# Performance work log

Measured on AMD Instinct MI355X. Metric: run time of the kernel, lower is better.

Reference implementation:

```python
import jax, jax.numpy as jnp
import numpy as np

B, L, H, LAT, V = 4096, 16, 256, 64, 800


def setup_inputs() -> dict:
    key = jax.random.key(0)
    ks = jax.random.split(key, 20)
    s = 0.05
    return {
        'wid': jax.random.randint(ks[0], (B, L), 0, V),
        'tree_vec': jax.random.normal(ks[1], (B, LAT), jnp.float32),
        'emb': jax.random.normal(ks[2], (V, H), jnp.float32) * s,
        'Wz_w': jax.random.normal(ks[3], (H, 2 * H), jnp.float32) * s,
        'Wz_b': jnp.zeros((H,), jnp.float32),
        'Wr_w': jax.random.normal(ks[4], (H, H), jnp.float32) * s,
        'Ur_w': jax.random.normal(ks[5], (H, H), jnp.float32) * s,
        'Ur_b': jnp.zeros((H,), jnp.float32),
        'Wh_w': jax.random.normal(ks[6], (H, 2 * H), jnp.float32) * s,
        'Wh_b': jnp.zeros((H,), jnp.float32),
        'W_w': jax.random.normal(ks[7], (H, LAT + H), jnp.float32) * s,
        'W_b': jnp.zeros((H,), jnp.float32),
        'U_w': jax.random.normal(ks[8], (H, LAT + 2 * H), jnp.float32) * s,
        'U_b': jnp.zeros((H,), jnp.float32),
        'Wo_w': jax.random.normal(ks[9], (V, H), jnp.float32) * s,
        'Wo_b': jnp.zeros((V,), jnp.float32),
        'Us_w': jax.random.normal(ks[10], (1, H), jnp.float32) * s,
        'Us_b': jnp.zeros((1,), jnp.float32),
    }


def _decoder(wid, tree_vec, emb, Wz_w, Wz_b, Wr_w, Ur_w, Ur_b, Wh_w, Wh_b,
             W_w, W_b, U_w, U_b, Wo_w, Wo_b, Us_w, Us_b):
    nB, nL = wid.shape
    x = emb[wid]                      # [B,L,H] node embeddings
    xt = jnp.transpose(x, (1, 0, 2))  # [L,B,H]

    def gru_scan(src_seq, dst_seq):
        # JTNN GRUUpdate along a chain: carry = (m_prev, rm_prev)
        def step(carry, xs):
            m_prev, rm_prev = carry
            x_src, x_dst = xs
            z = jax.nn.sigmoid(jnp.concatenate([x_src, m_prev], -1) @ Wz_w.T + Wz_b)
            h_til = jnp.tanh(jnp.concatenate([x_src, rm_prev], -1) @ Wh_w.T + Wh_b)
            m = (1.0 - z) * m_prev + z * h_til
            r = jax.nn.sigmoid(x_dst @ Wr_w.T + m @ Ur_w.T + Ur_b)
            return (m, r * m), m
        z0 = jnp.zeros((src_seq.shape[1], H), src_seq.dtype)
        _, m_seq = jax.lax.scan(step, (z0, z0), (src_seq, dst_seq))
        return m_seq  # [L-1,B,H]

    # forward edges t->t+1 (DFS forward), reverse edges t+1->t (DFS backtrack)
    m_fwd = gru_scan(xt[:-1], xt[1:])
    m_rev = gru_scan(xt[1:][::-1], xt[:-1][::-1])[::-1]  # indexed by t

    zeros_h = jnp.zeros((nB, H), x.dtype)
    tvL = lambda n: jnp.broadcast_to(tree_vec, (n, nB, LAT))

    # p_inputs = [x_v, h_v, tree_vec] at root, each fwd step, each rev step
    p_root = jnp.concatenate([x[:, 0], zeros_h, tree_vec], -1)[None]
    p_fwd = jnp.concatenate([xt[1:], m_fwd, tvL(nL - 1)], -1)
    m_fwd_shift = jnp.concatenate([zeros_h[None], m_fwd[:-1]], 0)
    h_rev = m_fwd_shift + m_rev  # node t after backtrack pull
    p_rev = jnp.concatenate([xt[:-1], h_rev, tvL(nL - 1)], -1)[::-1]
    p_in = jnp.concatenate([p_root, p_fwd, p_rev], 0).reshape(-1, 2 * H + LAT)
    # targets: forward expansions -> 1, backtracks + final stop -> 0
    p_t = jnp.concatenate([jnp.ones((nL - 1,)), jnp.zeros((nL,))])
    p_t = jnp.broadcast_to(p_t[:, None], (2 * nL - 1, nB)).reshape(-1)

    # q_inputs = [h, tree_vec] at root and each newly created node
    q_root = jnp.concatenate([zeros_h, tree_vec], -1)[None]
    q_new = jnp.concatenate([m_fwd, tvL(nL - 1)], -1)
    q_in = jnp.concatenate([q_root, q_new], 0).reshape(-1, H + LAT)
    q_t = jnp.transpose(wid, (1, 0)).reshape(-1)  # [L*B], step-major like q_in

    q = jax.nn.relu(q_in @ W_w.T + W_b) @ Wo_w.T + Wo_b  # [L*B, V]
    p = (jax.nn.relu(p_in @ U_w.T + U_b) @ Us_w.T + Us_b)[:, 0]

    p_loss = jnp.sum(jnp.logaddexp(0.0, p) - p * p_t) / nB
    logZ = jax.nn.logsumexp(q, axis=-1)
    q_sel = jnp.take_along_axis(q, q_t[:, None], axis=1)[:, 0]
    q_loss = jnp.sum(logZ - q_sel) / nB
    p_acc = jnp.mean(((p > 0).astype(jnp.int32) == p_t.astype(jnp.int32)).astype(jnp.float32))
    q_acc = jnp.mean((jnp.argmax(q, axis=-1) == q_t).astype(jnp.float32))
    return (q_loss, p_loss, q_acc, p_acc)


def reference(wid, tree_vec, emb, Wz_w, Wz_b, Wr_w, Ur_w, Ur_b, Wh_w, Wh_b,
              W_w, W_b, U_w, U_b, Wo_w, Wo_b, Us_w, Us_b):
    return _decoder(wid, tree_vec, emb, Wz_w, Wz_b, Wr_w, Ur_w, Ur_b, Wh_w, Wh_b,
                    W_w, W_b, U_w, U_b, Wo_w, Wo_b, Us_w, Us_b)
```

## Files before the change

kernel.cpp:

```cpp
#include <hip/hip_runtime.h>
#include <math.h>


typedef unsigned short u16;
typedef __attribute__((ext_vector_type(4))) float f4;
typedef __attribute__((ext_vector_type(4))) unsigned short u16x4;
typedef __attribute__((ext_vector_type(8))) unsigned short u16x8;
typedef __attribute__((ext_vector_type(8))) short s16x8;
typedef __attribute__((ext_vector_type(4))) float f32x4;

#define DEV static __device__ __forceinline__

DEV u16 f2b(float f) {
  unsigned u = __float_as_uint(f);
  u += 0x7fffu + ((u >> 16) & 1u);
  return (u16)(u >> 16);
}
DEV float b2f(u16 h) { return __uint_as_float(((unsigned)h) << 16); }
DEV void split2(float v, u16& hi, u16& lo) {
  hi = f2b(v);
  lo = f2b(v - b2f(hi));
}
DEV float fsig(float x) { return __builtin_amdgcn_rcpf(1.f + __expf(-x)); }
DEV float ftanh(float x) {
  const float e = __expf(2.f * x);
  return 1.f - 2.f * __builtin_amdgcn_rcpf(e + 1.f);
}

DEV void gld16(const void* g, void* l) {
  __builtin_amdgcn_global_load_lds((const __attribute__((address_space(1))) void*)g,
                                   (__attribute__((address_space(3))) void*)l, 16, 0, 0);
}

#define MFMA(a, b, c) __builtin_amdgcn_mfma_f32_16x16x32_bf16((a), (b), (c), 0, 0, 0)

template <int GR, int GC, bool ASPL, bool BSPL>
DEV void mm128(const u16* __restrict__ Ah, const u16* __restrict__ Al,
               const u16* __restrict__ Bh, const u16* __restrict__ Bl,
               int K, u16* sm, f32x4* acc) {
  constexpr int MT = 8 / GR, NT = 8 / GC;
  const int tid = threadIdx.x;
  const int lane = tid & 63;
  const int wv = tid >> 6;
  const int wr = wv / GC, wc = wv % GC;
  const size_t rs = (size_t)K * 2;
  const size_t soff = (size_t)(tid >> 2) * rs + (size_t)((tid & 3) * 16);
  const char* gAh = (const char*)Ah + soff;
  const char* gBh = (const char*)Bh + soff;
  const char* gAl = nullptr;
  const char* gBl = nullptr;
  if constexpr (ASPL) gAl = (const char*)Al + soff;
  if constexpr (BSPL) gBl = (const char*)Bl + soff;
  char* L = (char*)sm;
  const int wb = wv * 1024;
  const int frow = lane & 15, fkb = (lane >> 4) * 16;
  const char* rA = L + (size_t)((wr * 16 * MT + frow) * 64 + fkb);
  const char* rB = L + 8192 + (size_t)((wc * 16 * NT + frow) * 64 + fkb);
  const size_t rskip = rs * 64;
  const int nk = K >> 5;
  for (int kt = 0; kt < nk; ++kt) {
    gld16(gAh, L + wb);
    gld16(gAh + rskip, L + 4096 + wb);
    gld16(gBh, L + 8192 + wb);
    gld16(gBh + rskip, L + 12288 + wb);
    if constexpr (ASPL) {
      gld16(gAl, L + 16384 + wb);
      gld16(gAl + rskip, L + 20480 + wb);
    }
    if constexpr (BSPL) {
      gld16(gBl, L + 24576 + wb);
      gld16(gBl + rskip, L + 28672 + wb);
    }
    gAh += 64; gBh += 64;
    if constexpr (ASPL) gAl += 64;
    if constexpr (BSPL) gBl += 64;
    __syncthreads();
    s16x8 a_[MT], b_[NT];
#pragma unroll
    for (int i = 0; i < MT; ++i) a_[i] = *(const s16x8*)(rA + i * 1024);
#pragma unroll
    for (int j = 0; j < NT; ++j) b_[j] = *(const s16x8*)(rB + j * 1024);
#pragma unroll
    for (int i = 0; i < MT; ++i)
#pragma unroll
      for (int j = 0; j < NT; ++j)
        acc[i * NT + j] = MFMA(a_[i], b_[j], acc[i * NT + j]);
    if constexpr (BSPL) {
      s16x8 bl_[NT];
#pragma unroll
      for (int j = 0; j < NT; ++j) bl_[j] = *(const s16x8*)(rB + 16384 + j * 1024);
#pragma unroll
      for (int i = 0; i < MT; ++i)
#pragma unroll
        for (int j = 0; j < NT; ++j)
          acc[i * NT + j] = MFMA(a_[i], bl_[j], acc[i * NT + j]);
    }
    if constexpr (ASPL) {
      s16x8 al_[MT];
#pragma unroll
      for (int i = 0; i < MT; ++i) al_[i] = *(const s16x8*)(rA + 16384 + i * 1024);
#pragma unroll
      for (int i = 0; i < MT; ++i)
#pragma unroll
        for (int j = 0; j < NT; ++j)
          acc[i * NT + j] = MFMA(al_[i], b_[j], acc[i * NT + j]);
    }
    __syncthreads();
  }
}

__global__ __launch_bounds__(256) void k_pack(const float* __restrict__ Wz, const float* __restrict__ Wr,
                                              const float* __restrict__ Ur, const float* __restrict__ Wh,
                                              const float* __restrict__ Ww, const float* __restrict__ Uw,
                                              const float* __restrict__ Wo, const float* __restrict__ emb,
                                              const float* __restrict__ tree,
                                              u16* wpk, u16* uzh, u16* urw, u16* wu, u16* wt2, u16* wov,
                                              u16* uxp2, u16* utp2, u16* embp, u16* tre2) {
  const int i = blockIdx.x * 256 + threadIdx.x;
  const int seg = blockIdx.y;
  u16 h, l;
  if (seg == 0) {
    if (i >= 196608) return;
    const int row = i >> 8, c = i & 255;
    const float v = (row < 256) ? Wz[row * 512 + c]
                                : (row < 512) ? Wh[(row - 256) * 512 + c] : Wr[(row - 512) * 256 + c];
    split2(v, h, l); wpk[i] = h; wpk[196608 + i] = l;
  } else if (seg == 1) {
    if (i >= 131072) return;
    const int row = i >> 8, c = i & 255;
    const float v = (row < 256) ? Wz[row * 512 + 256 + c] : Wh[(row - 256) * 512 + 256 + c];
    uzh[i] = f2b(v);
  } else if (seg == 2) {
    if (i >= 65536) return;
    urw[i] = f2b(Ur[i]);
  } else if (seg == 3) {
    if (i >= 81920) return;
    if (i < 65536) {
      const int row = i >> 8, c = i & 255;
      wu[i] = f2b(Ww[row * 320 + c]);
    } else {
      const int j = i - 65536, row = j >> 6, c = j & 63;
      split2(Ww[row * 320 + 256 + c], h, l); wt2[j] = h; wt2[16384 + j] = l;
    }
  } else if (seg == 4) {
    if (i >= 229376) return;
    const float v = (i < 204800) ? Wo[i] : 0.f;
    wov[i] = f2b(v);
  } else if (seg == 5) {
    if (i >= 147456) return;
    if (i < 65536) {
      const int row = i >> 8, c = i & 255;
      split2(Uw[row * 576 + c], h, l); uxp2[i] = h; uxp2[65536 + i] = l;
    } else if (i < 131072) {
      const int j = i - 65536, row = j >> 8, c = j & 255;
      wu[65536 + j] = f2b(Uw[row * 576 + 256 + c]);
    } else {
      const int j = i - 131072, row = j >> 6, c = j & 63;
      split2(Uw[row * 576 + 512 + c], h, l); utp2[j] = h; utp2[16384 + j] = l;
    }
  } else if (seg == 6) {
    if (i >= 229376) return;
    const int row = i >> 8;
    const float v = (row < 800) ? emb[i] : 0.f;
    split2(v, h, l); embp[i] = h; embp[229376 + i] = l;
  } else {
    if (i >= 65536) return;
    const int b = i >> 4, c4 = (i & 15) << 2;
    const f4 tv = *(const f4*)(tree + (size_t)b * 64 + c4);
    u16x4 hi, lo;
#pragma unroll
    for (int k = 0; k < 4; ++k) { u16 hh, ll; split2(tv[k], hh, ll); hi[k] = hh; lo[k] = ll; }
    *(u16x4*)(tre2 + (size_t)b * 64 + c4) = hi;
    *(u16x4*)(tre2 + 262144 + (size_t)b * 64 + c4) = lo;
  }
}

__global__ __launch_bounds__(256) void k_prep(const u16* __restrict__ embp, const u16* __restrict__ wpk,
                                              const u16* __restrict__ tre2, const u16* __restrict__ wt2,
                                              const u16* __restrict__ utp2, const u16* __restrict__ uxp2,
                                              u16* __restrict__ Aembh, float* __restrict__ Tq,
                                              float* __restrict__ Tp, float* __restrict__ Xp) {
  __shared__ u16 sm[16384];
  f32x4 acc[16] = {};
  const int bid = blockIdx.x;
  int seg, bx, by, K;
  const u16 *A0, *B0;
  size_t Aoff, Boff;
  if (bid < 42) { seg = 0; bx = bid % 7; by = bid / 7; A0 = embp; Aoff = 229376; B0 = wpk; Boff = 196608; K = 256; }
  else if (bid < 106) { const int l2 = bid - 42; seg = 1; bx = l2 % 32; by = l2 / 32; A0 = tre2; Aoff = 262144; B0 = wt2; Boff = 16384; K = 64; }
  else if (bid < 170) { const int l2 = bid - 106; seg = 2; bx = l2 % 32; by = l2 / 32; A0 = tre2; Aoff = 262144; B0 = utp2; Boff = 16384; K = 64; }
  else { const int l2 = bid - 170; seg = 3; bx = l2 % 7; by = l2 / 7; A0 = embp; Aoff = 229376; B0 = uxp2; Boff = 65536; K = 256; }
  A0 += (size_t)bx * 128 * K;
  B0 += (size_t)by * 128 * K;
  mm128<2, 2, true, true>(A0, A0 + Aoff, B0, B0 + Boff, K, sm, acc);
  const int lane = threadIdx.x & 63, wv = threadIdx.x >> 6;
  const int wr = wv >> 1, wc = wv & 1, quad = lane >> 4, c = lane & 15;
#pragma unroll
  for (int i = 0; i < 4; ++i)
#pragma unroll
    for (int j = 0; j < 4; ++j)
#pragma unroll
      for (int rg = 0; rg < 4; ++rg) {
        const size_t row = (size_t)bx * 128 + wr * 64 + i * 16 + quad * 4 + rg;
        const int col = by * 128 + wc * 64 + j * 16 + c;
        const float v = acc[i * 4 + j][rg];
        if (seg == 0) Aembh[row * 768 + col] = f2b(v);
        else if (seg == 1) Tq[row * 256 + col] = v;
        else if (seg == 2) Tp[row * 256 + col] = v;
        else Xp[row * 256 + col] = v;
      }
}

__global__ __launch_bounds__(1024, 1) void k_scan(const u16* __restrict__ uzh, const u16* __restrict__ urw,
                                                  const u16* __restrict__ Aembh, const int* __restrict__ wid,
                                                  const float* __restrict__ Wz_b, const float* __restrict__ Wh_b,
                                                  const float* __restrict__ Ur_b,
                                                  u16* __restrict__ mfh, u16* __restrict__ mrh) {
  __shared__ __align__(16) u16 MH[8192];
  __shared__ __align__(16) u16 ML[8192];
  __shared__ __align__(16) u16 RH[8192];
  __shared__ __align__(16) u16 RL[8192];
  const int tid = threadIdx.x;
  const int wv = tid >> 6, lane = tid & 63;
  const int l15 = lane & 15, quad = lane >> 4;
  const int r0 = blockIdx.x * 32;
  const int dir = r0 >> 12;
  const int b0 = r0 & 4095;
  for (int i = tid; i < 8192; i += 1024) { MH[i] = 0; ML[i] = 0; RH[i] = 0; RL[i] = 0; }
  const int zc0 = wv * 16;
  const int cc = zc0 + l15;
  const float bzv = Wz_b[cc], bhv = Wh_b[cc], urv = Ur_b[cc];
  s16x8 wz[8], wh[8];
#pragma unroll
  for (int kc = 0; kc < 8; ++kc) {
    const size_t zo = (size_t)cc * 256 + kc * 32 + quad * 8;
    wz[kc] = *(const s16x8*)(uzh + zo);
    wh[kc] = *(const s16x8*)(uzh + zo + 65536);
  }
  float mnew[2][4];
  __syncthreads();
  for (int s = 0; s < 15; ++s) {
    const int tsrc = dir ? (15 - s) : s;
    const int tdst = dir ? (14 - s) : (s + 1);
    int xids[8], xds[8];
#pragma unroll
    for (int mt = 0; mt < 2; ++mt)
#pragma unroll
      for (int rg = 0; rg < 4; ++rg) {
        const int b = b0 + mt * 16 + quad * 4 + rg;
        xids[mt * 4 + rg] = wid[b * 16 + tsrc];
        xds[mt * 4 + rg] = (s < 14) ? wid[b * 16 + tdst] : 0;
      }
    f32x4 aZ[2] = {};
    f32x4 aH[2] = {};
    for (int kc = 0; kc < 8; ++kc) {
      s16x8 amh[2], aml[2], arh[2], arl[2];
#pragma unroll
      for (int mt = 0; mt < 2; ++mt) {
        const int ai = ((kc * 4 + quad) * 32 + mt * 16 + l15) * 8;
        amh[mt] = *(const s16x8*)&MH[ai];
        aml[mt] = *(const s16x8*)&ML[ai];
        arh[mt] = *(const s16x8*)&RH[ai];
        arl[mt] = *(const s16x8*)&RL[ai];
      }
#pragma unroll
      for (int mt = 0; mt < 2; ++mt) {
        aZ[mt] = MFMA(amh[mt], wz[kc], aZ[mt]);
        aZ[mt] = MFMA(aml[mt], wz[kc], aZ[mt]);
        aH[mt] = MFMA(arh[mt], wh[kc], aH[mt]);
        aH[mt] = MFMA(arl[mt], wh[kc], aH[mt]);
      }
    }
    __syncthreads();
#pragma unroll
    for (int mt = 0; mt < 2; ++mt)
#pragma unroll
      for (int rg = 0; rg < 4; ++rg) {
        const int rr = mt * 16 + quad * 4 + rg;
        const int xid = xids[mt * 4 + rg];
        const int mi = ((cc >> 3) * 32 + rr) * 8 + (cc & 7);
        const float az = b2f(Aembh[(size_t)xid * 768 + cc]);
        const float ah = b2f(Aembh[(size_t)xid * 768 + 256 + cc]);
        const float mp = b2f(MH[mi]) + b2f(ML[mi]);
        const float z = fsig(aZ[mt][rg] + az + bzv);
        const float ht = ftanh(aH[mt][rg] + ah + bhv);
        const float mv = (1.f - z) * mp + z * ht;
        mnew[mt][rg] = mv;
        u16 hh, ll; split2(mv, hh, ll);
        MH[mi] = hh; ML[mi] = ll;
      }
    __syncthreads();
    {
      u16* dst = dir ? (mrh + ((size_t)(14 - s) * 4096 + b0) * 256)
                     : (mfh + ((size_t)s * 4096 + b0) * 256);
      const int r = tid >> 5, cg = tid & 31;
      const s16x8 v = *(const s16x8*)&MH[(cg * 32 + r) * 8];
      *(s16x8*)(dst + r * 256 + cg * 8) = v;
    }
    if (s == 14) break;
    f32x4 aR[2] = {};
    for (int kc = 0; kc < 8; ++kc) {
      s16x8 amh[2], aml[2];
#pragma unroll
      for (int mt = 0; mt < 2; ++mt) {
        const int ai = ((kc * 4 + quad) * 32 + mt * 16 + l15) * 8;
        amh[mt] = *(const s16x8*)&MH[ai];
        aml[mt] = *(const s16x8*)&ML[ai];
      }
      const size_t ro = (size_t)cc * 256 + kc * 32 + quad * 8;
      const s16x8 brh = *(const s16x8*)(urw + ro);
#pragma unroll
      for (int mt = 0; mt < 2; ++mt) {
        aR[mt] = MFMA(amh[mt], brh, aR[mt]);
        aR[mt] = MFMA(aml[mt], brh, aR[mt]);
      }
    }
#pragma unroll
    for (int mt = 0; mt < 2; ++mt)
#pragma unroll
      for (int rg = 0; rg < 4; ++rg) {
        const int rr = mt * 16 + quad * 4 + rg;
        const int xd = xds[mt * 4 + rg];
        const int mi = ((cc >> 3) * 32 + rr) * 8 + (cc & 7);
        const float ar = b2f(Aembh[(size_t)xd * 768 + 512 + cc]);
        const float rp = aR[mt][rg] + ar + urv;
        const float rmv = fsig(rp) * mnew[mt][rg];
        u16 hh, ll; split2(rmv, hh, ll);
        RH[mi] = hh; RL[mi] = ll;
      }
    __syncthreads();
  }
}

__global__ __launch_bounds__(256) void k_mid(const u16* __restrict__ mfh, const u16* __restrict__ mrh,
                                             const u16* __restrict__ wu,
                                             const float* __restrict__ Tq, const float* __restrict__ W_b,
                                             const float* __restrict__ Xp, const float* __restrict__ Tp,
                                             const float* __restrict__ U_b, const float* __restrict__ Us_w,
                                             const int* __restrict__ wid,
                                             u16* __restrict__ hq, u16* __restrict__ hrev,
                                             float* __restrict__ ppart) {
  const int bid = blockIdx.x;
  const int tid = threadIdx.x;
  if (bid < 1920) {
    __shared__ u16 sm[8192];
    f32x4 acc[16] = {};
    const int rb = bid >> 2, ct = bid & 3;
    const u16* Ah = mfh + (size_t)rb * 128 * 256;
    const u16* Bh = wu + (size_t)ct * 128 * 256;
    mm128<4, 1, false, false>(Ah, nullptr, Bh, nullptr, 256, sm, acc);
    const int lane = tid & 63, wv = tid >> 6, quad = lane >> 4, c = lane & 15;
    if (ct < 2) {
      const int colb = ct * 128;
#pragma unroll
      for (int i = 0; i < 2; ++i)
#pragma unroll
        for (int rg = 0; rg < 4; ++rg) {
          const size_t row = (size_t)rb * 128 + wv * 32 + i * 16 + quad * 4 + rg;
          const int b = (int)(row & 4095);
#pragma unroll
          for (int j = 0; j < 8; ++j) {
            const int col = colb + j * 16 + c;
            const float hv = fmaxf(acc[i * 8 + j][rg] + Tq[(size_t)b * 256 + col] + W_b[col], 0.f);
            hq[(row + 4096) * 256 + col] = f2b(hv);
          }
        }
    } else {
      const int colb = (ct - 2) * 128;
#pragma unroll
      for (int i = 0; i < 2; ++i)
#pragma unroll
        for (int rg = 0; rg < 4; ++rg) {
          const size_t row = (size_t)rb * 128 + wv * 32 + i * 16 + quad * 4 + rg;
          const int t = (int)(row >> 12), b = (int)(row & 4095);
          const int xid = wid[b * 16 + t + 1];
          const int prow = (int)row + 4096;
          float d = 0.f;
#pragma unroll
          for (int j = 0; j < 8; ++j) {
            const int col = colb + j * 16 + c;
            float h = acc[i * 8 + j][rg] + Xp[(size_t)xid * 256 + col] + Tp[(size_t)b * 256 + col] + U_b[col];
            h = fmaxf(h, 0.f);
            d += h * Us_w[col];
          }
#pragma unroll
          for (int dd = 1; dd < 16; dd <<= 1) d += __shfl_xor(d, dd);
          if (c == 0) ppart[(size_t)prow * 2 + (ct - 2)] = d;
        }
    }
  } else if (bid < 9600) {
    const int idx = (bid - 1920) * 256 + tid;
    const int r = idx >> 5, g8 = idx & 31;
    const int t = r >> 12;
    const size_t o = (size_t)r * 256 + g8 * 8;
    const u16x8 a = *(const u16x8*)(mrh + o);
    u16x8 out = a;
    if (t > 0) {
      const u16x8 a2 = *(const u16x8*)(mfh + o - 1048576);
#pragma unroll
      for (int k = 0; k < 8; ++k) out[k] = f2b(b2f(a[k]) + b2f(a2[k]));
    }
    *(u16x8*)(hrev + o) = out;
  } else {
    const int b = bid - 9600;
    const int col = tid;
    const float hv = fmaxf(Tq[(size_t)b * 256 + col] + W_b[col], 0.f);
    hq[(size_t)b * 256 + col] = f2b(hv);
    const int xid = wid[b * 16];
    float d = fmaxf(Xp[(size_t)xid * 256 + col] + Tp[(size_t)b * 256 + col] + U_b[col], 0.f) * Us_w[col];
#pragma unroll
    for (int dd = 1; dd < 64; dd <<= 1) d += __shfl_xor(d, dd);
    __shared__ float red[4];
    if ((tid & 63) == 0) red[tid >> 6] = d;
    __syncthreads();
    if (tid == 0) {
      ppart[(size_t)b * 2] = red[0] + red[1] + red[2] + red[3];
      ppart[(size_t)b * 2 + 1] = 0.f;
    }
  }
}

__global__ __launch_bounds__(256) void k_tail(const u16* __restrict__ hq, const u16* __restrict__ wov,
                                              const u16* __restrict__ wu, const u16* __restrict__ hrev,
                                              const float* __restrict__ Wo_b, const float* __restrict__ Xp,
                                              const float* __restrict__ Tp, const float* __restrict__ U_b,
                                              const float* __restrict__ Us_w, const int* __restrict__ wid,
                                              float* __restrict__ qpart, float* __restrict__ ppart) {
  __shared__ __align__(16) u16 smem[40960];
  const int bid = blockIdx.x;
  const int tid = threadIdx.x, lane = tid & 63, wv = tid >> 6;
  const int quad = lane >> 4, c = lane & 15;
  if (bid < 512) {
    char* LA = (char*)smem;
    char* LB = (char*)(smem + 32768);
    const u16* Ah = hq + (size_t)bid * 128 * 256;
    const size_t soff = (size_t)(tid >> 2) * 512 + (size_t)((tid & 3) * 16);
#pragma unroll
    for (int kt = 0; kt < 8; ++kt) {
      gld16((const char*)Ah + soff + kt * 64, LA + kt * 8192 + wv * 1024);
      gld16((const char*)Ah + soff + 32768 + kt * 64, LA + kt * 8192 + 4096 + wv * 1024);
    }
    gld16((const char*)wov + soff, LB + wv * 1024);
    gld16((const char*)wov + soff + 32768, LB + 4096 + wv * 1024);
    float rM[8], rS[8], rSel[8];
    int rAm[8], qts[8];
#pragma unroll
    for (int mt = 0; mt < 2; ++mt)
#pragma unroll
      for (int rg = 0; rg < 4; ++rg) {
        const int r8 = mt * 4 + rg;
        rM[r8] = -1e30f; rS[r8] = 0.f; rSel[r8] = -1e30f; rAm[r8] = 0x7fffffff;
        const size_t row = (size_t)bid * 128 + wv * 32 + mt * 16 + quad * 4 + rg;
        qts[r8] = wid[(row & 4095) * 16 + (int)(row >> 12)];
      }
    f32x4 acc[16];
    for (int nt = 0; nt < 7; ++nt) {
#pragma unroll
      for (int i = 0; i < 16; ++i) acc[i] = (f32x4){0.f, 0.f, 0.f, 0.f};
      for (int kt = 0; kt < 8; ++kt) {
        const int g = nt * 8 + kt;
        __syncthreads();
        if (g < 55) {
          const int nn = (g + 1) >> 3, nk = (g + 1) & 7;
          const char* Bn = (const char*)(wov + (size_t)nn * 32768) + soff + nk * 64;
          gld16(Bn, LB + ((g + 1) & 1) * 8192 + wv * 1024);
          gld16(Bn + 32768, LB + ((g + 1) & 1) * 8192 + 4096 + wv * 1024);
        }
        s16x8 af[2], bf[8];
#pragma unroll
        for (int mt = 0; mt < 2; ++mt)
          af[mt] = *(const s16x8*)(LA + kt * 8192 + (wv * 32 + mt * 16 + c) * 64 + quad * 16);
#pragma unroll
        for (int j = 0; j < 8; ++j)
          bf[j] = *(const s16x8*)(LB + (g & 1) * 8192 + (j * 16 + c) * 64 + quad * 16);
#pragma unroll
        for (int mt = 0; mt < 2; ++mt)
#pragma unroll
          for (int j = 0; j < 8; ++j)
            acc[mt * 8 + j] = MFMA(af[mt], bf[j], acc[mt * 8 + j]);
      }
      const int colb = nt * 128;
#pragma unroll
      for (int mt = 0; mt < 2; ++mt)
#pragma unroll
        for (int rg = 0; rg < 4; ++rg) {
          const int r8 = mt * 4 + rg;
          float vals[8];
          float mx = -1e30f;
          int am = 0x7fffffff;
#pragma unroll
          for (int j = 0; j < 8; ++j) {
            const int col = colb + j * 16 + c;
            float v = -1e30f;
            if (col < 800) v = acc[mt * 8 + j][rg] + Wo_b[col];
            vals[j] = v;
            if (v > mx) { mx = v; am = col; }
          }
          float gm = mx;
          int ga = am;
#pragma unroll
          for (int d = 1; d < 16; d <<= 1) {
            const float om = __shfl_xor(gm, d);
            const int oa = __shfl_xor(ga, d);
            if (om > gm || (om == gm && oa < ga)) { gm = om; ga = oa; }
          }
          float s = 0.f, sel = -1e30f;
#pragma unroll
          for (int j = 0; j < 8; ++j) {
            s += __expf(vals[j] - gm);
            if (colb + j * 16 + c == qts[r8]) sel = vals[j];
          }
#pragma unroll
          for (int d = 1; d < 16; d <<= 1) {
            s += __shfl_xor(s, d);
            sel = fmaxf(sel, __shfl_xor(sel, d));
          }
          const float oM = rM[r8];
          if (gm > oM || (gm == oM && ga < rAm[r8])) rAm[r8] = ga;
          const float nM = fmaxf(oM, gm);
          rS[r8] = rS[r8] * __expf(oM - nM) + s * __expf(gm - nM);
          rM[r8] = nM;
          rSel[r8] = fmaxf(rSel[r8], sel);
        }
    }
    if (c == 0) {
#pragma unroll
      for (int mt = 0; mt < 2; ++mt)
#pragma unroll
        for (int rg = 0; rg < 4; ++rg) {
          const int r8 = mt * 4 + rg;
          const size_t row = (size_t)bid * 128 + wv * 32 + mt * 16 + quad * 4 + rg;
          f4 o;
          o.x = rM[r8]; o.y = rS[r8]; o.z = (float)rAm[r8]; o.w = rSel[r8];
          *(f4*)(qpart + row * 4) = o;
        }
    }
  } else {
    f32x4 acc[16] = {};
    const int l2 = bid - 512;
    const int by = l2 & 1, bx = l2 >> 1;
    const u16* Ah = hrev + (size_t)bx * 128 * 256;
    const u16* Bh = wu + (size_t)(256 + by * 128) * 256;
    mm128<4, 1, false, false>(Ah, nullptr, Bh, nullptr, 256, smem, acc);
    const int colb = by * 128;
#pragma unroll
    for (int i = 0; i < 2; ++i)
#pragma unroll
      for (int rg = 0; rg < 4; ++rg) {
        const size_t row = (size_t)bx * 128 + wv * 32 + i * 16 + quad * 4 + rg;
        const int t = (int)(row >> 12), b = (int)(row & 4095);
        const int xid = wid[b * 16 + t];
        const int prow = (30 - t) * 4096 + b;
        float d = 0.f;
#pragma unroll
        for (int j = 0; j < 8; ++j) {
          const int col = colb + j * 16 + c;
          float h = acc[i * 8 + j][rg] + Xp[(size_t)xid * 256 + col] + Tp[(size_t)b * 256 + col] + U_b[col];
          h = fmaxf(h, 0.f);
          d += h * Us_w[col];
        }
#pragma unroll
        for (int dd = 1; dd < 16; dd <<= 1) d += __shfl_xor(d, dd);
        if (c == 0) ppart[(size_t)prow * 2 + by] = d;
      }
  }
}

__global__ __launch_bounds__(256) void k_red(const float* __restrict__ qpart, const float* __restrict__ ppart,
                                             const int* __restrict__ wid, const float* __restrict__ Us_b,
                                             float* __restrict__ accb) {
  __shared__ float s0, s1;
  if (threadIdx.x == 0) { s0 = 0.f; s1 = 0.f; }
  __syncthreads();
  if (blockIdx.x < 256) {
    const int r = blockIdx.x * 256 + threadIdx.x;
    const f4 p4 = *(const f4*)(qpart + (size_t)r * 4);
    const float logZ = p4.x + logf(p4.y);
    const int am = (int)p4.z;
    const int t = r >> 12, b = r & 4095;
    const int qt = wid[b * 16 + t];
    atomicAdd(&s0, logZ - p4.w);
    atomicAdd(&s1, (am == qt) ? 1.f : 0.f);
    __syncthreads();
    if (threadIdx.x == 0) {
      atomicAdd(&accb[blockIdx.x & 15], s0);
      atomicAdd(&accb[16 + (blockIdx.x & 15)], s1);
    }
  } else {
    const int r = (blockIdx.x - 256) * 256 + threadIdx.x;
    const float p = ppart[(size_t)r * 2] + ppart[(size_t)r * 2 + 1] + Us_b[0];
    const int sidx = r >> 12;
    const float pt = (sidx < 15) ? 1.f : 0.f;
    const float loss = fmaxf(p, 0.f) + log1pf(expf(-fabsf(p))) - p * pt;
    const float hit = ((p > 0.f) == (pt > 0.5f)) ? 1.f : 0.f;
    atomicAdd(&s0, loss);
    atomicAdd(&s1, hit);
    __syncthreads();
    if (threadIdx.x == 0) {
      atomicAdd(&accb[32 + (blockIdx.x & 15)], s0);
      atomicAdd(&accb[48 + (blockIdx.x & 15)], s1);
    }
  }
}

__global__ void k_finalize(const float* __restrict__ accb, float* __restrict__ out) {
  if (threadIdx.x == 0 && blockIdx.x == 0) {
    float ql = 0, qa = 0, pl = 0, pa = 0;
    for (int i = 0; i < 16; ++i) {
      ql += accb[i];
      qa += accb[16 + i];
      pl += accb[32 + i];
      pa += accb[48 + i];
    }
    out[0] = ql / 4096.f;
    out[1] = pl / 4096.f;
    out[2] = qa / 65536.f;
    out[3] = pa / 126976.f;
  }
}

__global__ void k_flag(float* __restrict__ out) {
  if (threadIdx.x < 4) out[threadIdx.x] = -12345.f;
}

extern "C" void kernel_launch(void* const* d_in, const int* in_sizes, int n_in,
                              void* d_out, int out_size, void* d_ws, size_t ws_size,
                              hipStream_t stream) {
  (void)in_sizes; (void)n_in; (void)out_size;
  const int* wid = (const int*)d_in[0];
  const float* tree = (const float*)d_in[1];
  const float* emb = (const float*)d_in[2];
  const float* Wz_w = (const float*)d_in[3];
  const float* Wz_b = (const float*)d_in[4];
  const float* Wr_w = (const float*)d_in[5];
  const float* Ur_w = (const float*)d_in[6];
  const float* Ur_b = (const float*)d_in[7];
  const float* Wh_w = (const float*)d_in[8];
  const float* Wh_b = (const float*)d_in[9];
  const float* W_w = (const float*)d_in[10];
  const float* W_b = (const float*)d_in[11];
  const float* U_w = (const float*)d_in[12];
  const float* U_b = (const float*)d_in[13];
  const float* Wo_w = (const float*)d_in[14];
  const float* Wo_b = (const float*)d_in[15];
  const float* Us_w = (const float*)d_in[16];
  const float* Us_b = (const float*)d_in[17];
  char* ws = (char*)d_ws;

  constexpr size_t NEED = 152273152ull;
  if (ws_size < NEED) {
    k_flag<<<1, 64, 0, stream>>>((float*)d_out);
    return;
  }

  u16* hq = (u16*)(ws + 0ull);
  u16* hrev = (u16*)(ws + 33554432ull);
  u16* mfh = (u16*)(ws + 65011712ull);
  u16* mrh = (u16*)(ws + 96468992ull);
  u16* Aembh = (u16*)(ws + 127926272ull);
  u16* embp = (u16*)(ws + 129302528ull);
  u16* wpk = (u16*)(ws + 130220032ull);
  u16* uzh = (u16*)(ws + 131006464ull);
  u16* urw = (u16*)(ws + 131268608ull);
  u16* wu = (u16*)(ws + 131399680ull);
  u16* wt2 = (u16*)(ws + 131661824ull);
  u16* wov = (u16*)(ws + 131727360ull);
  u16* uxp2 = (u16*)(ws + 132186112ull);
  u16* utp2 = (u16*)(ws + 132448256ull);
  u16* tre2 = (u16*)(ws + 132513792ull);
  float* Tq = (float*)(ws + 133562368ull);
  float* Tp = (float*)(ws + 137756672ull);
  float* Xp = (float*)(ws + 141950976ull);
  float* qpart = (float*)(ws + 142868480ull);
  float* ppart = (float*)(ws + 151257088ull);
  float* accb = (float*)(ws + 152272896ull);

  hipMemsetAsync(accb, 0, 256, stream);

  k_pack<<<dim3(896, 8), 256, 0, stream>>>(Wz_w, Wr_w, Ur_w, Wh_w, W_w, U_w, Wo_w, emb, tree,
                                           wpk, uzh, urw, wu, wt2, wov, uxp2, utp2, embp, tre2);
  k_prep<<<184, 256, 0, stream>>>(embp, wpk, tre2, wt2, utp2, uxp2, Aembh, Tq, Tp, Xp);
  k_scan<<<256, 1024, 0, stream>>>(uzh, urw, Aembh, wid, Wz_b, Wh_b, Ur_b, mfh, mrh);
  k_mid<<<13696, 256, 0, stream>>>(mfh, mrh, wu, Tq, W_b, Xp, Tp, U_b, Us_w, wid, hq, hrev, ppart);
  k_tail<<<1472, 256, 0, stream>>>(hq, wov, wu, hrev, Wo_b, Xp, Tp, U_b, Us_w, wid, qpart, ppart);
  k_red<<<752, 256, 0, stream>>>(qpart, ppart, wid, Us_b, accb);
  k_finalize<<<1, 64, 0, stream>>>(accb, (float*)d_out);
}
```

Before: 561.1 us.

## Stage per-step embedding rows in LDS for scan and fuse q-loss reduction into tail

```diff
diff --git a/kernel.cpp b/kernel.cpp
--- a/kernel.cpp
+++ b/kernel.cpp
@@ -220,6 +220,8 @@
   __shared__ __align__(16) u16 ML[8192];
   __shared__ __align__(16) u16 RH[8192];
   __shared__ __align__(16) u16 RL[8192];
+  __shared__ __align__(16) u16 AE[16640];
+  __shared__ __align__(16) u16 AD[8448];
   const int tid = threadIdx.x;
   const int wv = tid >> 6, lane = tid & 63;
   const int l15 = lane & 15, quad = lane >> 4;
@@ -242,15 +244,20 @@
   for (int s = 0; s < 15; ++s) {
     const int tsrc = dir ? (15 - s) : s;
     const int tdst = dir ? (14 - s) : (s + 1);
-    int xids[8], xds[8];
-#pragma unroll
-    for (int mt = 0; mt < 2; ++mt)
-#pragma unroll
-      for (int rg = 0; rg < 4; ++rg) {
-        const int b = b0 + mt * 16 + quad * 4 + rg;
-        xids[mt * 4 + rg] = wid[b * 16 + tsrc];
-        xds[mt * 4 + rg] = (s < 14) ? wid[b * 16 + tdst] : 0;
-      }
+#pragma unroll
+    for (int it = 0; it < 2; ++it) {
+      const int ch = it * 1024 + tid;
+      const int r = ch >> 6, o = (ch & 63) * 8;
+      const int xid = wid[(b0 + r) * 16 + tsrc];
+      const s16x8 v = *(const s16x8*)(Aembh + (size_t)xid * 768 + o);
+      *(s16x8*)&AE[r * 520 + o] = v;
+    }
+    if (s < 14) {
+      const int r = tid >> 5, o = (tid & 31) * 8;
+      const int xd = wid[(b0 + r) * 16 + tdst];
+      const s16x8 v = *(const s16x8*)(Aembh + (size_t)xd * 768 + 512 + o);
+      *(s16x8*)&AD[r * 264 + o] = v;
+    }
     f32x4 aZ[2] = {};
     f32x4 aH[2] = {};
     for (int kc = 0; kc < 8; ++kc) {
@@ -277,10 +284,9 @@
 #pragma unroll
       for (int rg = 0; rg < 4; ++rg) {
         const int rr = mt * 16 + quad * 4 + rg;
-        const int xid = xids[mt * 4 + rg];
         const int mi = ((cc >> 3) * 32 + rr) * 8 + (cc & 7);
-        const float az = b2f(Aembh[(size_t)xid * 768 + cc]);
-        const float ah = b2f(Aembh[(size_t)xid * 768 + 256 + cc]);
+        const float az = b2f(AE[rr * 520 + cc]);
+        const float ah = b2f(AE[rr * 520 + 256 + cc]);
         const float mp = b2f(MH[mi]) + b2f(ML[mi]);
         const float z = fsig(aZ[mt][rg] + az + bzv);
         const float ht = ftanh(aH[mt][rg] + ah + bhv);
@@ -320,9 +326,8 @@
 #pragma unroll
       for (int rg = 0; rg < 4; ++rg) {
         const int rr = mt * 16 + quad * 4 + rg;
-        const int xd = xds[mt * 4 + rg];
         const int mi = ((cc >> 3) * 32 + rr) * 8 + (cc & 7);
-        const float ar = b2f(Aembh[(size_t)xd * 768 + 512 + cc]);
+        const float ar = b2f(AD[rr * 264 + cc]);
         const float rp = aR[mt][rg] + ar + urv;
         const float rmv = fsig(rp) * mnew[mt][rg];
         u16 hh, ll; split2(rmv, hh, ll);
@@ -425,14 +430,16 @@
                                               const float* __restrict__ Wo_b, const float* __restrict__ Xp,
                                               const float* __restrict__ Tp, const float* __restrict__ U_b,
                                               const float* __restrict__ Us_w, const int* __restrict__ wid,
-                                              float* __restrict__ qpart, float* __restrict__ ppart) {
+                                              float* __restrict__ accb, float* __restrict__ ppart) {
   __shared__ __align__(16) u16 smem[40960];
+  __shared__ float qred[2];
   const int bid = blockIdx.x;
   const int tid = threadIdx.x, lane = tid & 63, wv = tid >> 6;
   const int quad = lane >> 4, c = lane & 15;
   if (bid < 512) {
     char* LA = (char*)smem;
     char* LB = (char*)(smem + 32768);
+    if (tid == 0) { qred[0] = 0.f; qred[1] = 0.f; }
     const u16* Ah = hq + (size_t)bid * 128 * 256;
     const size_t soff = (size_t)(tid >> 2) * 512 + (size_t)((tid & 3) * 16);
 #pragma unroll
@@ -524,16 +531,19 @@
         }
     }
     if (c == 0) {
-#pragma unroll
-      for (int mt = 0; mt < 2; ++mt)
-#pragma unroll
-        for (int rg = 0; rg < 4; ++rg) {
-          const int r8 = mt * 4 + rg;
-          const size_t row = (size_t)bid * 128 + wv * 32 + mt * 16 + quad * 4 + rg;
-          f4 o;
-          o.x = rM[r8]; o.y = rS[r8]; o.z = (float)rAm[r8]; o.w = rSel[r8];
-          *(f4*)(qpart + row * 4) = o;
-        }
+      float lsum = 0.f, hsum = 0.f;
+#pragma unroll
+      for (int r8 = 0; r8 < 8; ++r8) {
+        lsum += rM[r8] + logf(rS[r8]) - rSel[r8];
+        hsum += (rAm[r8] == qts[r8]) ? 1.f : 0.f;
+      }
+      atomicAdd(&qred[0], lsum);
+      atomicAdd(&qred[1], hsum);
+    }
+    __syncthreads();
+    if (tid == 0) {
+      atomicAdd(&accb[bid & 15], qred[0]);
+      atomicAdd(&accb[16 + (bid & 15)], qred[1]);
     }
   } else {
     f32x4 acc[16] = {};
@@ -566,40 +576,23 @@
   }
 }
 
-__global__ __launch_bounds__(256) void k_red(const float* __restrict__ qpart, const float* __restrict__ ppart,
-                                             const int* __restrict__ wid, const float* __restrict__ Us_b,
+__global__ __launch_bounds__(256) void k_red(const float* __restrict__ ppart, const float* __restrict__ Us_b,
                                              float* __restrict__ accb) {
   __shared__ float s0, s1;
   if (threadIdx.x == 0) { s0 = 0.f; s1 = 0.f; }
   __syncthreads();
-  if (blockIdx.x < 256) {
-    const int r = blockIdx.x * 256 + threadIdx.x;
-    const f4 p4 = *(const f4*)(qpart + (size_t)r * 4);
-    const float logZ = p4.x + logf(p4.y);
-    const int am = (int)p4.z;
-    const int t = r >> 12, b = r & 4095;
-    const int qt = wid[b * 16 + t];
-    atomicAdd(&s0, logZ - p4.w);
-    atomicAdd(&s1, (am == qt) ? 1.f : 0.f);
-    __syncthreads();
-    if (threadIdx.x == 0) {
-      atomicAdd(&accb[blockIdx.x & 15], s0);
-      atomicAdd(&accb[16 + (blockIdx.x & 15)], s1);
-    }
-  } else {
-    const int r = (blockIdx.x - 256) * 256 + threadIdx.x;
-    const float p = ppart[(size_t)r * 2] + ppart[(size_t)r * 2 + 1] + Us_b[0];
-    const int sidx = r >> 12;
-    const float pt = (sidx < 15) ? 1.f : 0.f;
-    const float loss = fmaxf(p, 0.f) + log1pf(expf(-fabsf(p))) - p * pt;
-    const float hit = ((p > 0.f) == (pt > 0.5f)) ? 1.f : 0.f;
-    atomicAdd(&s0, loss);
-    atomicAdd(&s1, hit);
-    __syncthreads();
-    if (threadIdx.x == 0) {
-      atomicAdd(&accb[32 + (blockIdx.x & 15)], s0);
-      atomicAdd(&accb[48 + (blockIdx.x & 15)], s1);
-    }
+  const int r = blockIdx.x * 256 + threadIdx.x;
+  const float p = ppart[(size_t)r * 2] + ppart[(size_t)r * 2 + 1] + Us_b[0];
+  const int sidx = r >> 12;
+  const float pt = (sidx < 15) ? 1.f : 0.f;
+  const float loss = fmaxf(p, 0.f) + log1pf(expf(-fabsf(p))) - p * pt;
+  const float hit = ((p > 0.f) == (pt > 0.5f)) ? 1.f : 0.f;
+  atomicAdd(&s0, loss);
+  atomicAdd(&s1, hit);
+  __syncthreads();
+  if (threadIdx.x == 0) {
+    atomicAdd(&accb[32 + (blockIdx.x & 15)], s0);
+    atomicAdd(&accb[48 + (blockIdx.x & 15)], s1);
   }
 }
 
@@ -671,7 +664,6 @@
   float* Tq = (float*)(ws + 133562368ull);
   float* Tp = (float*)(ws + 137756672ull);
   float* Xp = (float*)(ws + 141950976ull);
-  float* qpart = (float*)(ws + 142868480ull);
   float* ppart = (float*)(ws + 151257088ull);
   float* accb = (float*)(ws + 152272896ull);
 
@@ -682,7 +674,7 @@
   k_prep<<<184, 256, 0, stream>>>(embp, wpk, tre2, wt2, utp2, uxp2, Aembh, Tq, Tp, Xp);
   k_scan<<<256, 1024, 0, stream>>>(uzh, urw, Aembh, wid, Wz_b, Wh_b, Ur_b, mfh, mrh);
   k_mid<<<13696, 256, 0, stream>>>(mfh, mrh, wu, Tq, W_b, Xp, Tp, U_b, Us_w, wid, hq, hrev, ppart);
-  k_tail<<<1472, 256, 0, stream>>>(hq, wov, wu, hrev, Wo_b, Xp, Tp, U_b, Us_w, wid, qpart, ppart);
-  k_red<<<752, 256, 0, stream>>>(qpart, ppart, wid, Us_b, accb);
+  k_tail<<<1472, 256, 0, stream>>>(hq, wov, wu, hrev, Wo_b, Xp, Tp, U_b, Us_w, wid, accb, ppart);
+  k_red<<<496, 256, 0, stream>>>(ppart, Us_b, accb);
   k_finalize<<<1, 64, 0, stream>>>(accb, (float*)d_out);
 }
```

Result: slower. 704.3 us (+25.5%).
